# Optimization experiments

Hardware: AMD Instinct MI355X
Metric: run time of the kernel (lower is better)

## Reference

```python
import jax, jax.numpy as jnp
import numpy as np


def setup_inputs() -> dict:
    key = jax.random.key(0)
    k1, k2, k3 = jax.random.split(key, 3)
    B, S, V, D = 2, 128, 1024, 512
    x = jax.random.normal(k1, (B, S, V, D), dtype=jnp.float32)
    W1 = jax.random.normal(k2, (32, D), dtype=jnp.float32) * (1.0 / np.sqrt(D))
    b1 = jnp.zeros((32,), dtype=jnp.float32)
    W2 = jax.random.normal(k3, (1, 32), dtype=jnp.float32) * (1.0 / np.sqrt(32))
    b2 = jnp.zeros((1,), dtype=jnp.float32)
    return {"x": x, "W1": W1, "b1": b1, "W2": W2, "b2": b2}


def reference(x, W1, b1, W2, b2):
    # x: [B, S, V, D]. Original transposes to [B, V, S, D]; we keep layout and
    # adjust axes, which is the same math.
    h = jnp.einsum('bsvd,kd->bsvk', x, W1) + b1          # [B,S,V,32]
    score = jnp.einsum('bsvk,ok->bsvo', h, W2) + b2      # [B,S,V,1]
    score = score[..., 0]                                # [B,S,V]
    w = jax.nn.softmax(score, axis=1)                    # softmax over seq_len
    out = jnp.einsum('bsv,bsvd->bvd', w, x)              # [B,V,D]
    return out
```

## Files before the change

kernel.cpp:

```cpp
#include <hip/hip_runtime.h>
#include <math.h>


#define BB 2
#define SS 128
#define VV 1024
#define DD 512
#define KK 32
#define WPB 4
#define SW (SS / WPB)

__global__ __launch_bounds__(128) void weff_kernel(
    const float* __restrict__ W1, const float* __restrict__ W2,
    float* __restrict__ weff)
{
    const int d = blockIdx.x * 128 + threadIdx.x;
    float acc = 0.f;
#pragma unroll
    for (int k = 0; k < KK; ++k)
        acc = fmaf(W2[k], W1[k * DD + d], acc);
    weff[d] = acc;
}

__global__ __launch_bounds__(256) void node_attn_kernel(
    const float* __restrict__ x, const float* __restrict__ weff,
    float* __restrict__ out)
{
    const int lane = threadIdx.x & 63;
    const int w    = threadIdx.x >> 6;
    const int pair = blockIdx.x;
    const int b = pair >> 10;
    const int v = pair & (VV - 1);
    const int d0 = lane * 4;
    const int d1 = 256 + lane * 4;

    const float4 wl = *(const float4*)(weff + d0);
    const float4 wh = *(const float4*)(weff + d1);

    const size_t sstr = (size_t)VV * DD;
    const float* xp = x + (size_t)b * SS * sstr + (size_t)v * DD
                        + (size_t)(w * SW) * sstr;

    float4 bl[4], bh[4];
#pragma unroll
    for (int i = 0; i < 4; ++i) {
        bl[i] = *(const float4*)(xp + (size_t)i * sstr + d0);
        bh[i] = *(const float4*)(xp + (size_t)i * sstr + d1);
    }

    float  l  = 0.f;
    float4 ol = make_float4(0.f, 0.f, 0.f, 0.f);
    float4 oh = make_float4(0.f, 0.f, 0.f, 0.f);

    for (int s = 0; s < SW; s += 2) {
        const float4 c0l = bl[s & 3],      c0h = bh[s & 3];
        const float4 c1l = bl[(s + 1) & 3], c1h = bh[(s + 1) & 3];
        if (s + 4 < SW) {
            const float* p0 = xp + (size_t)(s + 4) * sstr;
            const float* p1 = xp + (size_t)(s + 5) * sstr;
            bl[s & 3]       = *(const float4*)(p0 + d0);
            bh[s & 3]       = *(const float4*)(p0 + d1);
            bl[(s + 1) & 3] = *(const float4*)(p1 + d0);
            bh[(s + 1) & 3] = *(const float4*)(p1 + d1);
        }

        float t0 = c0l.x * wl.x + c0l.y * wl.y + c0l.z * wl.z + c0l.w * wl.w
                 + c0h.x * wh.x + c0h.y * wh.y + c0h.z * wh.z + c0h.w * wh.w;
        float t1 = c1l.x * wl.x + c1l.y * wl.y + c1l.z * wl.z + c1l.w * wl.w
                 + c1h.x * wh.x + c1h.y * wh.y + c1h.z * wh.z + c1h.w * wh.w;
#pragma unroll
        for (int off = 32; off > 0; off >>= 1) {
            t0 += __shfl_xor(t0, off, 64);
            t1 += __shfl_xor(t1, off, 64);
        }
        const float p0 = __expf(t0);
        const float p1 = __expf(t1);
        l += p0 + p1;
        ol.x = fmaf(p0, c0l.x, fmaf(p1, c1l.x, ol.x));
        ol.y = fmaf(p0, c0l.y, fmaf(p1, c1l.y, ol.y));
        ol.z = fmaf(p0, c0l.z, fmaf(p1, c1l.z, ol.z));
        ol.w = fmaf(p0, c0l.w, fmaf(p1, c1l.w, ol.w));
        oh.x = fmaf(p0, c0h.x, fmaf(p1, c1h.x, oh.x));
        oh.y = fmaf(p0, c0h.y, fmaf(p1, c1h.y, oh.y));
        oh.z = fmaf(p0, c0h.z, fmaf(p1, c1h.z, oh.z));
        oh.w = fmaf(p0, c0h.w, fmaf(p1, c1h.w, oh.w));
    }

    __shared__ float osh[WPB][DD];
    __shared__ float lsh[WPB];
    *(float4*)(&osh[w][d0]) = ol;
    *(float4*)(&osh[w][d1]) = oh;
    if (lane == 0) lsh[w] = l;
    __syncthreads();

    const int t = threadIdx.x;
    const float lt  = lsh[0] + lsh[1] + lsh[2] + lsh[3];
    const float inv = 1.0f / lt;
    float sx = 0.f, sy = 0.f;
#pragma unroll
    for (int q = 0; q < WPB; ++q) {
        sx += osh[q][t * 2];
        sy += osh[q][t * 2 + 1];
    }
    float* op = out + ((size_t)b * VV + v) * DD;
    *(float2*)(op + t * 2) = make_float2(sx * inv, sy * inv);
}

extern "C" void kernel_launch(void* const* d_in, const int* in_sizes, int n_in,
                              void* d_out, int out_size, void* d_ws, size_t ws_size,
                              hipStream_t stream) {
    const float* x  = (const float*)d_in[0];
    const float* W1 = (const float*)d_in[1];
    const float* W2 = (const float*)d_in[3];
    float* out  = (float*)d_out;
    float* weff = (float*)d_ws;

    weff_kernel<<<dim3(DD / 128), dim3(128), 0, stream>>>(W1, W2, weff);
    node_attn_kernel<<<dim3(BB * VV), dim3(256), 0, stream>>>(x, weff, out);
}
```

Baseline: 690.4 us.

## Fuse W2·W1 effective-weight computation into main kernel and unroll seq loop

```diff
diff --git a/kernel.cpp b/kernel.cpp
--- a/kernel.cpp
+++ b/kernel.cpp
@@ -10,21 +10,11 @@
 #define WPB 4
 #define SW (SS / WPB)
 
-__global__ __launch_bounds__(128) void weff_kernel(
-    const float* __restrict__ W1, const float* __restrict__ W2,
-    float* __restrict__ weff)
-{
-    const int d = blockIdx.x * 128 + threadIdx.x;
-    float acc = 0.f;
-#pragma unroll
-    for (int k = 0; k < KK; ++k)
-        acc = fmaf(W2[k], W1[k * DD + d], acc);
-    weff[d] = acc;
-}
+typedef float f4 __attribute__((ext_vector_type(4)));
 
 __global__ __launch_bounds__(256) void node_attn_kernel(
-    const float* __restrict__ x, const float* __restrict__ weff,
-    float* __restrict__ out)
+    const float* __restrict__ x, const float* __restrict__ W1,
+    const float* __restrict__ W2, float* __restrict__ out)
 {
     const int lane = threadIdx.x & 63;
     const int w    = threadIdx.x >> 6;
@@ -34,34 +24,47 @@
     const int d0 = lane * 4;
     const int d1 = 256 + lane * 4;
 
-    const float4 wl = *(const float4*)(weff + d0);
-    const float4 wh = *(const float4*)(weff + d1);
-
     const size_t sstr = (size_t)VV * DD;
     const float* xp = x + (size_t)b * SS * sstr + (size_t)v * DD
                         + (size_t)(w * SW) * sstr;
 
-    float4 bl[4], bh[4];
+    f4 bl[4], bh[4];
 #pragma unroll
     for (int i = 0; i < 4; ++i) {
-        bl[i] = *(const float4*)(xp + (size_t)i * sstr + d0);
-        bh[i] = *(const float4*)(xp + (size_t)i * sstr + d1);
+        bl[i] = *(const f4*)(xp + (size_t)i * sstr + d0);
+        bh[i] = *(const f4*)(xp + (size_t)i * sstr + d1);
     }
 
-    float  l  = 0.f;
-    float4 ol = make_float4(0.f, 0.f, 0.f, 0.f);
-    float4 oh = make_float4(0.f, 0.f, 0.f, 0.f);
+    f4 wl = 0.f, wh = 0.f;
+#pragma unroll 4
+    for (int k = 0; k < KK; ++k) {
+        const float w2k = W2[k];
+        const f4 a = *(const f4*)(W1 + (size_t)k * DD + d0);
+        const f4 c = *(const f4*)(W1 + (size_t)k * DD + d1);
+        wl.x = fmaf(w2k, a.x, wl.x);
+        wl.y = fmaf(w2k, a.y, wl.y);
+        wl.z = fmaf(w2k, a.z, wl.z);
+        wl.w = fmaf(w2k, a.w, wl.w);
+        wh.x = fmaf(w2k, c.x, wh.x);
+        wh.y = fmaf(w2k, c.y, wh.y);
+        wh.z = fmaf(w2k, c.z, wh.z);
+        wh.w = fmaf(w2k, c.w, wh.w);
+    }
 
+    float l = 0.f;
+    f4 ol = 0.f, oh = 0.f;
+
+#pragma unroll
     for (int s = 0; s < SW; s += 2) {
-        const float4 c0l = bl[s & 3],      c0h = bh[s & 3];
-        const float4 c1l = bl[(s + 1) & 3], c1h = bh[(s + 1) & 3];
+        const f4 c0l = bl[s & 3],       c0h = bh[s & 3];
+        const f4 c1l = bl[(s + 1) & 3], c1h = bh[(s + 1) & 3];
         if (s + 4 < SW) {
             const float* p0 = xp + (size_t)(s + 4) * sstr;
             const float* p1 = xp + (size_t)(s + 5) * sstr;
-            bl[s & 3]       = *(const float4*)(p0 + d0);
-            bh[s & 3]       = *(const float4*)(p0 + d1);
-            bl[(s + 1) & 3] = *(const float4*)(p1 + d0);
-            bh[(s + 1) & 3] = *(const float4*)(p1 + d1);
+            bl[s & 3]       = *(const f4*)(p0 + d0);
+            bh[s & 3]       = *(const f4*)(p0 + d1);
+            bl[(s + 1) & 3] = *(const f4*)(p1 + d0);
+            bh[(s + 1) & 3] = *(const f4*)(p1 + d1);
         }
 
         float t0 = c0l.x * wl.x + c0l.y * wl.y + c0l.z * wl.z + c0l.w * wl.w
@@ -88,8 +91,8 @@
 
     __shared__ float osh[WPB][DD];
     __shared__ float lsh[WPB];
-    *(float4*)(&osh[w][d0]) = ol;
-    *(float4*)(&osh[w][d1]) = oh;
+    *(f4*)(&osh[w][d0]) = ol;
+    *(f4*)(&osh[w][d1]) = oh;
     if (lane == 0) lsh[w] = l;
     __syncthreads();
 
@@ -113,8 +116,7 @@
     const float* W1 = (const float*)d_in[1];
     const float* W2 = (const float*)d_in[3];
     float* out  = (float*)d_out;
-    float* weff = (float*)d_ws;
+    (void)d_ws; (void)ws_size;
 
-    weff_kernel<<<dim3(DD / 128), dim3(128), 0, stream>>>(W1, W2, weff);
-    node_attn_kernel<<<dim3(BB * VV), dim3(256), 0, stream>>>(x, weff, out);
+    node_attn_kernel<<<dim3(BB * VV), dim3(256), 0, stream>>>(x, W1, W2, out);
 }
```

After: 676.3 us. -2.0%, faster.
